# Optimization experiments

Hardware: AMD Instinct MI355X
Metric: run time of the kernel (lower is better)

Reference implementation:

```python
import jax, jax.numpy as jnp
import numpy as np

N = 100000   # nodes
E = 500000   # edges
H = 128      # h_dim
TAU = 1.0    # gumbel-softmax temperature (module default)


def setup_inputs() -> dict:
    key = jax.random.key(0)
    k = jax.random.split(key, 6)
    h = jax.random.normal(k[0], (N, H), dtype=jnp.float32)
    W1 = jax.random.normal(k[1], (2 * H, H // 2), dtype=jnp.float32) / np.float32(np.sqrt(2 * H))
    b1 = jnp.zeros((H // 2,), dtype=jnp.float32)
    W2 = jax.random.normal(k[2], (H // 2, 1), dtype=jnp.float32) / np.float32(np.sqrt(H // 2))
    b2 = jnp.zeros((1,), dtype=jnp.float32)
    u = jax.random.uniform(k[3], (E, 2), dtype=jnp.float32, minval=1e-6, maxval=1.0)
    edge_index = jax.random.randint(k[4], (2, E), 0, N, dtype=jnp.int32)
    return {"h": h, "W1": W1, "b1": b1, "W2": W2, "b2": b2, "u": u, "edge_index": edge_index}


def reference(h, W1, b1, W2, b2, u, edge_index):
    row, col = edge_index[0], edge_index[1]
    # gather endpoint features and concat: [E, 2H]
    edge_feat = jnp.concatenate([h[row], h[col]], axis=-1)
    # 2-layer MLP scorer -> per-edge logit [E]
    hid = jax.nn.relu(edge_feat @ W1 + b1)
    logits = (hid @ W2 + b2)[:, 0]
    # binary gumbel-softmax over [keep-logit=0, logit]
    samp_logits = jnp.stack([jnp.zeros_like(logits), logits], axis=-1)  # [E, 2]
    g = -jnp.log(-jnp.log(u))  # gumbel noise from uniform
    y_soft = jax.nn.softmax((samp_logits + g) / TAU, axis=-1)
    # hard=True straight-through
    idx = jnp.argmax(y_soft, axis=-1)
    y_hard = jax.nn.one_hot(idx, 2, dtype=y_soft.dtype)
    y = y_hard - jax.lax.stop_gradient(y_soft) + y_soft
    weights = y[:, 1]
    return (weights, logits)
```

## Files before the change

kernel.cpp:

```cpp
#include <hip/hip_runtime.h>
#include <math.h>

#define NN 100000
#define NE 500000

__global__ __launch_bounds__(256, 2)
void node_proj(const float* __restrict__ h, const float* __restrict__ W1,
               const float* __restrict__ b1, float* __restrict__ AB, int nnodes)
{
    __shared__ float lw[32 * 128];
    __shared__ float lh[128 * 36];

    const int t   = threadIdx.x;
    const int tj  = t & 15;
    const int tnf = t >> 4;
    const int n0  = blockIdx.x * 128;

    float acc[8][8];
#pragma unroll
    for (int r = 0; r < 8; ++r)
#pragma unroll
        for (int j = 0; j < 8; ++j) acc[r][j] = 0.f;

    for (int kc = 0; kc < 4; ++kc) {
#pragma unroll
        for (int i = 0; i < 4; ++i) {
            int cid = t + 256 * i;
            int kl  = cid >> 5;
            int q   = cid & 31;
            int jo  = q * 4;
            int kg  = kc * 32 + kl;
            const float* src = (jo < 64) ? (W1 + kg * 64 + jo)
                                         : (W1 + (128 + kg) * 64 + (jo - 64));
            float4 v = *(const float4*)src;
            *(float4*)&lw[kl * 128 + jo] = v;
        }
#pragma unroll
        for (int i = 0; i < 4; ++i) {
            int cid = t + 256 * i;
            int nl  = cid >> 3;
            int kq  = cid & 7;
            int ng  = n0 + nl;
            float4 v = make_float4(0.f, 0.f, 0.f, 0.f);
            if (ng < nnodes) v = *(const float4*)&h[ng * 128 + kc * 32 + kq * 4];
            *(float4*)&lh[nl * 36 + kq * 4] = v;
        }
        __syncthreads();

#pragma unroll
        for (int k4 = 0; k4 < 8; ++k4) {
            float hv[8][4];
#pragma unroll
            for (int r = 0; r < 8; ++r) {
                float4 x = *(const float4*)&lh[(tnf + 16 * r) * 36 + k4 * 4];
                hv[r][0] = x.x; hv[r][1] = x.y; hv[r][2] = x.z; hv[r][3] = x.w;
            }
#pragma unroll
            for (int kk = 0; kk < 4; ++kk) {
                float4 wa = *(const float4*)&lw[(k4 * 4 + kk) * 128 + tj * 4];
                float4 wb = *(const float4*)&lw[(k4 * 4 + kk) * 128 + 64 + tj * 4];
#pragma unroll
                for (int r = 0; r < 8; ++r) {
                    float hval = hv[r][kk];
                    acc[r][0] += hval * wa.x;
                    acc[r][1] += hval * wa.y;
                    acc[r][2] += hval * wa.z;
                    acc[r][3] += hval * wa.w;
                    acc[r][4] += hval * wb.x;
                    acc[r][5] += hval * wb.y;
                    acc[r][6] += hval * wb.z;
                    acc[r][7] += hval * wb.w;
                }
            }
        }
        __syncthreads();
    }

    float4 bva = *(const float4*)&b1[tj * 4];
#pragma unroll
    for (int r = 0; r < 8; ++r) {
        int ng = n0 + tnf + 16 * r;
        if (ng >= nnodes) continue;
        float4 o1 = make_float4(acc[r][0] + bva.x, acc[r][1] + bva.y,
                                acc[r][2] + bva.z, acc[r][3] + bva.w);
        float4 o2 = make_float4(acc[r][4], acc[r][5], acc[r][6], acc[r][7]);
        *(float4*)&AB[ng * 128 + tj * 4]      = o1;
        *(float4*)&AB[ng * 128 + 64 + tj * 4] = o2;
    }
}

__global__ __launch_bounds__(256)
void edge_sample(const float* __restrict__ AB, const float* __restrict__ W2,
                 const float* __restrict__ b2, const float* __restrict__ u,
                 const int* __restrict__ ei, float* __restrict__ out)
{
    int t = threadIdx.x;
    int l = t & 15;
    int e = blockIdx.x * 16 + (t >> 4);

    int row = ei[e];
    int col = ei[NE + e];

    float4 a = *(const float4*)&AB[row * 128 + l * 4];
    float4 b = *(const float4*)&AB[col * 128 + 64 + l * 4];
    float4 w = *(const float4*)&W2[l * 4];

    float h0 = fmaxf(a.x + b.x, 0.f);
    float h1 = fmaxf(a.y + b.y, 0.f);
    float h2 = fmaxf(a.z + b.z, 0.f);
    float h3 = fmaxf(a.w + b.w, 0.f);

    float p = h0 * w.x + h1 * w.y + h2 * w.z + h3 * w.w;
    p += __shfl_xor(p, 1);
    p += __shfl_xor(p, 2);
    p += __shfl_xor(p, 4);
    p += __shfl_xor(p, 8);

    if (l == 0) {
        float logit = p + b2[0];
        float u0 = u[2 * e];
        float u1 = u[2 * e + 1];
        float g0 = -logf(-logf(u0));
        float g1 = -logf(-logf(u1));
        out[e]      = (logit + g1 > g0) ? 1.0f : 0.0f;
        out[NE + e] = logit;
    }
}

__global__ __launch_bounds__(256)
void edge_direct(const float* __restrict__ h, const float* __restrict__ W1,
                 const float* __restrict__ b1, const float* __restrict__ W2,
                 const float* __restrict__ b2, const float* __restrict__ u,
                 const int* __restrict__ ei, float* __restrict__ out)
{
    int t = threadIdx.x;
    int l = t & 15;
    int e = blockIdx.x * 16 + (t >> 4);

    int row = ei[e];
    int col = ei[NE + e];

    float a0 = 0.f, a1 = 0.f, a2 = 0.f, a3 = 0.f;
    const float* hr = h + (size_t)row * 128;
    const float* hc = h + (size_t)col * 128;

    for (int k4 = 0; k4 < 32; ++k4) {
        float4 hv = *(const float4*)&hr[k4 * 4];
#pragma unroll
        for (int kk = 0; kk < 4; ++kk) {
            float4 wr = *(const float4*)&W1[(k4 * 4 + kk) * 64 + l * 4];
            float hval = (&hv.x)[kk];
            a0 += hval * wr.x; a1 += hval * wr.y; a2 += hval * wr.z; a3 += hval * wr.w;
        }
    }
    for (int k4 = 0; k4 < 32; ++k4) {
        float4 hv = *(const float4*)&hc[k4 * 4];
#pragma unroll
        for (int kk = 0; kk < 4; ++kk) {
            float4 wr = *(const float4*)&W1[(128 + k4 * 4 + kk) * 64 + l * 4];
            float hval = (&hv.x)[kk];
            a0 += hval * wr.x; a1 += hval * wr.y; a2 += hval * wr.z; a3 += hval * wr.w;
        }
    }
    float4 bb = *(const float4*)&b1[l * 4];
    float4 w  = *(const float4*)&W2[l * 4];
    float h0 = fmaxf(a0 + bb.x, 0.f);
    float h1 = fmaxf(a1 + bb.y, 0.f);
    float h2 = fmaxf(a2 + bb.z, 0.f);
    float h3 = fmaxf(a3 + bb.w, 0.f);

    float p = h0 * w.x + h1 * w.y + h2 * w.z + h3 * w.w;
    p += __shfl_xor(p, 1);
    p += __shfl_xor(p, 2);
    p += __shfl_xor(p, 4);
    p += __shfl_xor(p, 8);

    if (l == 0) {
        float logit = p + b2[0];
        float u0 = u[2 * e];
        float u1 = u[2 * e + 1];
        float g0 = -logf(-logf(u0));
        float g1 = -logf(-logf(u1));
        out[e]      = (logit + g1 > g0) ? 1.0f : 0.0f;
        out[NE + e] = logit;
    }
}

extern "C" void kernel_launch(void* const* d_in, const int* in_sizes, int n_in,
                              void* d_out, int out_size, void* d_ws, size_t ws_size,
                              hipStream_t stream)
{
    const float* h  = (const float*)d_in[0];
    const float* W1 = (const float*)d_in[1];
    const float* b1 = (const float*)d_in[2];
    const float* W2 = (const float*)d_in[3];
    const float* b2 = (const float*)d_in[4];
    const float* u  = (const float*)d_in[5];
    const int*   ei = (const int*)d_in[6];
    float* out = (float*)d_out;

    const size_t need = (size_t)NN * 128 * sizeof(float);
    if (ws_size >= need) {
        float* AB = (float*)d_ws;
        int nblocks = (NN + 127) / 128;
        node_proj<<<nblocks, 256, 0, stream>>>(h, W1, b1, AB, NN);
        edge_sample<<<NE / 16, 256, 0, stream>>>(AB, W2, b2, u, ei, out);
    } else {
        edge_direct<<<NE / 16, 256, 0, stream>>>(h, W1, b1, W2, b2, u, ei, out);
    }
}
```

Measured before the change: 97.16 us.

## Compute node projection with one thread per node and uniform weight loads

The tiled shared-memory GEMM in node_proj is replaced by a one-thread-per-node scheme. Each thread keeps 128 accumulators in registers, streams its own row of h with a one-step prefetch, and reads W1 through wave-uniform loads. This drops the shared-memory staging and the block barriers. In exchange each thread needs very high register pressure (128 accumulators plus temporaries), the h row reads are strided across lanes so they coalesce poorly, and the output writes are also strided per thread, all of which can lower occupancy and bandwidth efficiency.

```diff
diff --git a/kernel.cpp b/kernel.cpp
--- a/kernel.cpp
+++ b/kernel.cpp
@@ -4,88 +4,65 @@
 #define NN 100000
 #define NE 500000
 
-__global__ __launch_bounds__(256, 2)
+__global__ __launch_bounds__(256)
 void node_proj(const float* __restrict__ h, const float* __restrict__ W1,
                const float* __restrict__ b1, float* __restrict__ AB, int nnodes)
 {
-    __shared__ float lw[32 * 128];
-    __shared__ float lh[128 * 36];
+    const int n = blockIdx.x * 256 + threadIdx.x;
+    const bool valid = (n < nnodes);
 
-    const int t   = threadIdx.x;
-    const int tj  = t & 15;
-    const int tnf = t >> 4;
-    const int n0  = blockIdx.x * 128;
+    float acc[128];
+#pragma unroll
+    for (int q = 0; q < 16; ++q) {
+        float4 bv = *(const float4*)&b1[q * 4];
+        acc[q * 4 + 0] = bv.x; acc[q * 4 + 1] = bv.y;
+        acc[q * 4 + 2] = bv.z; acc[q * 4 + 3] = bv.w;
+    }
+#pragma unroll
+    for (int j = 64; j < 128; ++j) acc[j] = 0.f;
 
-    float acc[8][8];
+    const float* hrow = h + (size_t)n * 128;
+    float4 hv = valid ? *(const float4*)&hrow[0] : make_float4(0.f, 0.f, 0.f, 0.f);
+
+#pragma unroll 1
+    for (int k4 = 0; k4 < 32; ++k4) {
+        float4 hnext = (valid && k4 < 31) ? *(const float4*)&hrow[(k4 + 1) * 4]
+                                          : make_float4(0.f, 0.f, 0.f, 0.f);
 #pragma unroll
-    for (int r = 0; r < 8; ++r)
+        for (int kk = 0; kk < 4; ++kk) {
+            const int k = k4 * 4 + kk;
+            const float4* wa = (const float4*)(W1 + k * 64);
+            const float4* wb = (const float4*)(W1 + (128 + k) * 64);
+            const float hk = (kk == 0) ? hv.x : (kk == 1) ? hv.y
+                           : (kk == 2) ? hv.z : hv.w;
 #pragma unroll
-        for (int j = 0; j < 8; ++j) acc[r][j] = 0.f;
-
-    for (int kc = 0; kc < 4; ++kc) {
-#pragma unroll
-        for (int i = 0; i < 4; ++i) {
-            int cid = t + 256 * i;
-            int kl  = cid >> 5;
-            int q   = cid & 31;
-            int jo  = q * 4;
-            int kg  = kc * 32 + kl;
-            const float* src = (jo < 64) ? (W1 + kg * 64 + jo)
-                                         : (W1 + (128 + kg) * 64 + (jo - 64));
-            float4 v = *(const float4*)src;
-            *(float4*)&lw[kl * 128 + jo] = v;
-        }
-#pragma unroll
-        for (int i = 0; i < 4; ++i) {
-            int cid = t + 256 * i;
-            int nl  = cid >> 3;
-            int kq  = cid & 7;
-            int ng  = n0 + nl;
-            float4 v = make_float4(0.f, 0.f, 0.f, 0.f);
-            if (ng < nnodes) v = *(const float4*)&h[ng * 128 + kc * 32 + kq * 4];
-            *(float4*)&lh[nl * 36 + kq * 4] = v;
-        }
-        __syncthreads();
-
-#pragma unroll
-        for (int k4 = 0; k4 < 8; ++k4) {
-            float hv[8][4];
-#pragma unroll
-            for (int r = 0; r < 8; ++r) {
-                float4 x = *(const float4*)&lh[(tnf + 16 * r) * 36 + k4 * 4];
-                hv[r][0] = x.x; hv[r][1] = x.y; hv[r][2] = x.z; hv[r][3] = x.w;
+            for (int q = 0; q < 16; ++q) {
+                float4 w4 = wa[q];
+                acc[q * 4 + 0] += hk * w4.x;
+                acc[q * 4 + 1] += hk * w4.y;
+                acc[q * 4 + 2] += hk * w4.z;
+                acc[q * 4 + 3] += hk * w4.w;
             }
 #pragma unroll
-            for (int kk = 0; kk < 4; ++kk) {
-                float4 wa = *(const float4*)&lw[(k4 * 4 + kk) * 128 + tj * 4];
-                float4 wb = *(const float4*)&lw[(k4 * 4 + kk) * 128 + 64 + tj * 4];
-#pragma unroll
-                for (int r = 0; r < 8; ++r) {
-                    float hval = hv[r][kk];
-                    acc[r][0] += hval * wa.x;
-                    acc[r][1] += hval * wa.y;
-                    acc[r][2] += hval * wa.z;
-                    acc[r][3] += hval * wa.w;
-                    acc[r][4] += hval * wb.x;
-                    acc[r][5] += hval * wb.y;
-                    acc[r][6] += hval * wb.z;
-                    acc[r][7] += hval * wb.w;
-                }
+            for (int q = 0; q < 16; ++q) {
+                float4 w4 = wb[q];
+                acc[64 + q * 4 + 0] += hk * w4.x;
+                acc[64 + q * 4 + 1] += hk * w4.y;
+                acc[64 + q * 4 + 2] += hk * w4.z;
+                acc[64 + q * 4 + 3] += hk * w4.w;
             }
         }
-        __syncthreads();
+        hv = hnext;
     }
 
-    float4 bva = *(const float4*)&b1[tj * 4];
+    if (valid) {
+        float* orow = AB + (size_t)n * 128;
 #pragma unroll
-    for (int r = 0; r < 8; ++r) {
-        int ng = n0 + tnf + 16 * r;
-        if (ng >= nnodes) continue;
-        float4 o1 = make_float4(acc[r][0] + bva.x, acc[r][1] + bva.y,
-                                acc[r][2] + bva.z, acc[r][3] + bva.w);
-        float4 o2 = make_float4(acc[r][4], acc[r][5], acc[r][6], acc[r][7]);
-        *(float4*)&AB[ng * 128 + tj * 4]      = o1;
-        *(float4*)&AB[ng * 128 + 64 + tj * 4] = o2;
+        for (int q = 0; q < 32; ++q) {
+            float4 o = make_float4(acc[q * 4 + 0], acc[q * 4 + 1],
+                                   acc[q * 4 + 2], acc[q * 4 + 3]);
+            *(float4*)&orow[q * 4] = o;
+        }
     }
 }
 
@@ -101,8 +78,8 @@
     int row = ei[e];
     int col = ei[NE + e];
 
-    float4 a = *(const float4*)&AB[row * 128 + l * 4];
-    float4 b = *(const float4*)&AB[col * 128 + 64 + l * 4];
+    float4 a = *(const float4*)&AB[(size_t)row * 128 + l * 4];
+    float4 b = *(const float4*)&AB[(size_t)col * 128 + 64 + l * 4];
     float4 w = *(const float4*)&W2[l * 4];
 
     float h0 = fmaxf(a.x + b.x, 0.f);
@@ -202,7 +179,7 @@
     const size_t need = (size_t)NN * 128 * sizeof(float);
     if (ws_size >= need) {
         float* AB = (float*)d_ws;
-        int nblocks = (NN + 127) / 128;
+        int nblocks = (NN + 255) / 256;
         node_proj<<<nblocks, 256, 0, stream>>>(h, W1, b1, AB, NN);
         edge_sample<<<NE / 16, 256, 0, stream>>>(AB, W2, b2, u, ei, out);
     } else {
```

Result: slower. 167.0 us (+71.9%).
